# Kernel tuning notes

Measured on AMD Instinct MI355X. Metric: run time of the kernel, lower is better.

Reference implementation:

```python
import jax, jax.numpy as jnp
import numpy as np

B, S, HID = 2, 2048, 2048
N_HEADS, N_KV, HEAD_DIM = 8, 1, 256
ROPE_THETA = 10000.0
NEG = -1e9


def setup_inputs() -> dict:
    key = jax.random.key(0)
    ks = jax.random.split(key, 6)
    hidden_states = jax.random.normal(ks[0], (B, S, HID), dtype=jnp.float32)
    position_ids = jnp.broadcast_to(jnp.arange(S, dtype=jnp.int32)[None, :], (B, S))
    causal = jnp.tril(jnp.ones((S, S), dtype=bool))
    attention_mask = jnp.where(causal, 0.0, NEG).astype(jnp.float32)[None, None]
    attention_mask = jnp.broadcast_to(attention_mask, (B, 1, S, S))
    sc = 0.02
    Wq = jax.random.normal(ks[1], (N_HEADS * HEAD_DIM, HID), dtype=jnp.float32) * sc
    Wk = jax.random.normal(ks[2], (N_KV * HEAD_DIM, HID), dtype=jnp.float32) * sc
    Wv = jax.random.normal(ks[3], (N_KV * HEAD_DIM, HID), dtype=jnp.float32) * sc
    Wo = jax.random.normal(ks[4], (HID, N_HEADS * HEAD_DIM), dtype=jnp.float32) * sc
    return {"hidden_states": hidden_states, "position_ids": position_ids,
            "attention_mask": attention_mask, "Wq": Wq, "Wk": Wk, "Wv": Wv, "Wo": Wo}


def _rotate_half(x):
    x1, x2 = jnp.split(x, 2, axis=-1)
    return jnp.concatenate((-x2, x1), axis=-1)


def _rope_cos_sin(position_ids, head_dim, dtype):
    inv_freq = 1.0 / (ROPE_THETA ** (jnp.arange(0, head_dim, 2, dtype=jnp.float32) / head_dim))
    freqs = position_ids.astype(jnp.float32)[:, :, None] * inv_freq[None, None, :]  # [B,S,D/2]
    emb = jnp.concatenate((freqs, freqs), axis=-1)  # [B,S,D]
    return jnp.cos(emb).astype(dtype), jnp.sin(emb).astype(dtype)


def reference(hidden_states, position_ids, attention_mask, Wq, Wk, Wv, Wo):
    b, s, _ = hidden_states.shape
    d = HEAD_DIM
    rep = N_HEADS // N_KV
    q = (hidden_states @ Wq.T).reshape(b, s, N_HEADS, d).transpose(0, 2, 1, 3)  # [B,H,S,D]
    k = (hidden_states @ Wk.T).reshape(b, s, N_KV, d).transpose(0, 2, 1, 3)    # [B,KV,S,D]
    v = (hidden_states @ Wv.T).reshape(b, s, N_KV, d).transpose(0, 2, 1, 3)
    cos, sin = _rope_cos_sin(position_ids, d, hidden_states.dtype)
    cos, sin = cos[:, None], sin[:, None]  # broadcast over heads
    q = q * cos + _rotate_half(q) * sin
    k = k * cos + _rotate_half(k) * sin
    # GQA: group queries per kv head, no materialized repeat
    qg = q.reshape(b, N_KV, rep, s, d)
    scores = jnp.einsum('bgrqd,bgkd->bgrqk', qg, k) / jnp.sqrt(jnp.float32(d)).astype(q.dtype)
    scores = scores.reshape(b, N_HEADS, s, s) + attention_mask
    probs = jax.nn.softmax(scores.astype(jnp.float32), axis=-1).astype(q.dtype)
    out = jnp.einsum('bgrqk,bgkd->bgrqd', probs.reshape(b, N_KV, rep, s, s), v)
    out = out.reshape(b, N_HEADS, s, d).transpose(0, 2, 1, 3).reshape(b, s, N_HEADS * d)
    return out @ Wo.T
```

## Files before the change

### kernel.cpp

```cpp
#include <hip/hip_runtime.h>
#include <hip/hip_bf16.h>

typedef __bf16 bf16x8 __attribute__((ext_vector_type(8)));
typedef float  f32x4  __attribute__((ext_vector_type(4)));

#define BATCH 2
#define SEQ   2048
#define HID   2048
#define NH    8
#define DH    256
#define LQ    2560
#define ROWS  (BATCH*SEQ)
#define KVB   32
#define NQC   128

__device__ __forceinline__ void gld16(const void* g, void* l) {
    __builtin_amdgcn_global_load_lds(
        (__attribute__((address_space(1))) void*)(g),
        (__attribute__((address_space(3))) void*)(l), 16, 0, 0);
}

__device__ __forceinline__ unsigned pack2bf(float a, float b) {
    union { __bf16 h[2]; unsigned u; } x;
    x.h[0] = (__bf16)a; x.h[1] = (__bf16)b;
    return x.u;
}

__global__ void cvt_f32_bf16(const float* __restrict__ src, __bf16* __restrict__ dst, int n4) {
    int i = blockIdx.x * blockDim.x + threadIdx.x;
    if (i < n4) {
        float4 v = ((const float4*)src)[i];
        __bf16 o[4];
        o[0] = (__bf16)v.x; o[1] = (__bf16)v.y; o[2] = (__bf16)v.z; o[3] = (__bf16)v.w;
        ((uint2*)dst)[i] = *(uint2*)o;
    }
}

template<typename CT>
__global__ __launch_bounds__(256)
void gemm_bt(const __bf16* __restrict__ A, const __bf16* __restrict__ B,
             CT* __restrict__ C, int M, int N, int K) {
    __shared__ __bf16 sA[128 * 32];
    __shared__ __bf16 sB[128 * 32];
    const int tid  = threadIdx.x;
    const int lane = tid & 63;
    const int wid  = tid >> 6;
    const int row0 = blockIdx.y * 128;
    const int col0 = blockIdx.x * 128;
    const int wr = (wid >> 1) * 64;
    const int wc = (wid & 1) * 64;

    const int sr0 = tid >> 2, sc0 = (tid & 3) * 8;
    const __bf16* Ag0 = A + (size_t)(row0 + sr0) * K + sc0;
    const __bf16* Ag1 = Ag0 + (size_t)64 * K;
    const __bf16* Bg0 = B + (size_t)(col0 + sr0) * K + sc0;
    const __bf16* Bg1 = Bg0 + (size_t)64 * K;
    __bf16* lA0 = &sA[wid * 512];
    __bf16* lA1 = &sA[2048 + wid * 512];
    __bf16* lB0 = &sB[wid * 512];
    __bf16* lB1 = &sB[2048 + wid * 512];

    f32x4 acc[4][4];
#pragma unroll
    for (int m = 0; m < 4; ++m)
#pragma unroll
        for (int n = 0; n < 4; ++n) acc[m][n] = (f32x4)0.f;

    for (int k0 = 0; k0 < K; k0 += 32) {
        gld16(Ag0 + k0, lA0);
        gld16(Ag1 + k0, lA1);
        gld16(Bg0 + k0, lB0);
        gld16(Bg1 + k0, lB1);
        __syncthreads();
        bf16x8 af[4], bfr[4];
#pragma unroll
        for (int m = 0; m < 4; ++m)
            af[m] = *(const bf16x8*)&sA[(wr + m * 16 + (lane & 15)) * 32 + (lane >> 4) * 8];
#pragma unroll
        for (int n = 0; n < 4; ++n)
            bfr[n] = *(const bf16x8*)&sB[(wc + n * 16 + (lane & 15)) * 32 + (lane >> 4) * 8];
#pragma unroll
        for (int m = 0; m < 4; ++m)
#pragma unroll
            for (int n = 0; n < 4; ++n)
                acc[m][n] = __builtin_amdgcn_mfma_f32_16x16x32_bf16(af[m], bfr[n], acc[m][n], 0, 0, 0);
        __syncthreads();
    }
#pragma unroll
    for (int m = 0; m < 4; ++m)
#pragma unroll
        for (int n = 0; n < 4; ++n)
#pragma unroll
            for (int r = 0; r < 4; ++r) {
                int row = row0 + wr + m * 16 + (lane >> 4) * 4 + r;
                int col = col0 + wc + n * 16 + (lane & 15);
                C[(size_t)row * N + col] = (CT)acc[m][n][r];
            }
}

__global__ void rope_kernel(__bf16* __restrict__ QKV, const int* __restrict__ pid) {
    const int row = blockIdx.x;
    const int h   = blockIdx.y;
    const int j   = threadIdx.x;
    const float pos = (float)pid[row];
    const float freq = exp2f((float)j * (-13.287712379549449f / 128.0f));
    const float ang = pos * freq;
    float sn, cs;
    sincosf(ang, &sn, &cs);
    __bf16* p = QKV + (size_t)row * LQ + h * 256 + j;
    float x1 = (float)p[0], x2 = (float)p[128];
    p[0]   = (__bf16)(x1 * cs - x2 * sn);
    p[128] = (__bf16)(x2 * cs + x1 * sn);
}

__global__ __launch_bounds__(256)
void transpose_v(const __bf16* __restrict__ QKV, __bf16* __restrict__ Vt) {
    __shared__ __bf16 t[32][33];
    const int b  = blockIdx.z;
    const int s0 = blockIdx.x * 32;
    const int d0 = blockIdx.y * 32;
    const int c  = threadIdx.x & 31;
    const int r8 = threadIdx.x >> 5;
#pragma unroll
    for (int i = 0; i < 4; ++i) {
        int row = r8 + i * 8;
        t[row][c] = QKV[(size_t)(b * SEQ + s0 + row) * LQ + 2304 + d0 + c];
    }
    __syncthreads();
#pragma unroll
    for (int i = 0; i < 4; ++i) {
        int row = r8 + i * 8;
        Vt[((size_t)b * 256 + d0 + row) * SEQ + s0 + c] = t[c][row];
    }
}

__global__ __launch_bounds__(128, 2)
void attn_fwd2(const __bf16* __restrict__ QKV, const __bf16* __restrict__ Vt,
               __bf16* __restrict__ O) {
    __shared__ __bf16 Kt[2][KVB * 256];
    __shared__ __bf16 Vs[2][256 * KVB];

    const int tid  = threadIdx.x;
    const int lane = tid & 63;
    const int wid  = tid >> 6;
    const int lc   = lane & 15;
    const int l4   = lane >> 4;

    const int bid = blockIdx.x;
    const int hg  = bid & 3;
    const int p   = bid >> 2;
    const int b   = p >> 6;
    const int pr  = p & 63;
    const int h   = hg * 2 + wid;

    const char* QKVb = (const char*)(QKV + (size_t)(b * SEQ) * LQ);
    const char* Kg   = QKVb + 2048 * 2;
    const char* Vg   = (const char*)(Vt + (size_t)b * DH * SEQ);

    const int krow = wid * 16 + (lane >> 5);
    const int kcol = (lane & 31) * 16;
    const int vrow = wid * 128 + (lane >> 2);
    const int vcol = (lane & 3) * 16;

    for (int half = 0; half < 2; ++half) {
        const int qt = half ? (NQC - 1 - pr) : pr;
        const int q0 = qt * 16;
        const int nt = (qt >> 1) + 1;
        const int qrow = q0 + lc;

        const char* Qp = QKVb + (size_t)(q0 + lc) * (LQ * 2) + h * 512 + l4 * 16;
        bf16x8 qf[8];
#pragma unroll
        for (int kc = 0; kc < 8; ++kc) qf[kc] = *(const bf16x8*)(Qp + kc * 64);

        f32x4 oacc[16];
#pragma unroll
        for (int i = 0; i < 16; ++i) oacc[i] = (f32x4)0.f;
        float mrow = -1e30f, lrow = 0.f;

#pragma unroll
        for (int i = 0; i < 8; ++i) {
            int r = krow + i * 2;
            gld16(Kg + (size_t)r * (LQ * 2) + (kcol ^ ((r & 7) << 4)),
                  (char*)&Kt[0][0] + wid * 8192 + i * 1024);
        }
#pragma unroll
        for (int i = 0; i < 8; ++i) {
            int r = vrow + i * 16;
            gld16(Vg + (size_t)r * (SEQ * 2) + vcol,
                  (char*)&Vs[0][0] + wid * 8192 + i * 1024);
        }

        int buf = 0;
        for (int t = 0; t < nt; ++t) {
            __syncthreads();
            const int kv0 = t * KVB;
            if (t + 1 < nt) {
                const int kvn = kv0 + KVB;
#pragma unroll
                for (int i = 0; i < 8; ++i) {
                    int r = krow + i * 2;
                    gld16(Kg + (size_t)(kvn + r) * (LQ * 2) + (kcol ^ ((r & 7) << 4)),
                          (char*)&Kt[buf ^ 1][0] + wid * 8192 + i * 1024);
                }
#pragma unroll
                for (int i = 0; i < 8; ++i) {
                    int r = vrow + i * 16;
                    gld16(Vg + (size_t)r * (SEQ * 2) + kvn * 2 + vcol,
                          (char*)&Vs[buf ^ 1][0] + wid * 8192 + i * 1024);
                }
            }

            f32x4 sacc[2];
            sacc[0] = (f32x4)0.f; sacc[1] = (f32x4)0.f;
            const char* Kl = (const char*)&Kt[buf][0];
#pragma unroll
            for (int ct = 0; ct < 2; ++ct) {
                const int rr = ct * 16 + lc;
                const int rbase = rr * 512;
                const int sw = (rr & 7) << 4;
#pragma unroll
                for (int kc = 0; kc < 8; ++kc) {
                    bf16x8 kf = *(const bf16x8*)(Kl + rbase + (((kc << 6) | (l4 << 4)) ^ sw));
                    sacc[ct] = __builtin_amdgcn_mfma_f32_16x16x32_bf16(kf, qf[kc], sacc[ct], 0, 0, 0);
                }
            }

            const bool lastt = (t == nt - 1);
            float sv[2][4];
            float rm = -1e30f;
#pragma unroll
            for (int ct = 0; ct < 2; ++ct)
#pragma unroll
                for (int r = 0; r < 4; ++r) {
                    float s = sacc[ct][r] * 0.0625f;
                    if (lastt) {
                        int kv = kv0 + ct * 16 + l4 * 4 + r;
                        if (kv > qrow) s = -1e30f;
                    }
                    sv[ct][r] = s;
                    rm = fmaxf(rm, s);
                }
            rm = fmaxf(rm, __shfl_xor(rm, 16, 64));
            rm = fmaxf(rm, __shfl_xor(rm, 32, 64));
            const float mnew  = fmaxf(mrow, rm);
            const float alpha = __expf(mrow - mnew);
            mrow = mnew;
            float p0[4], p1[4], ps = 0.f;
#pragma unroll
            for (int r = 0; r < 4; ++r) { p0[r] = __expf(sv[0][r] - mnew); ps += p0[r]; }
#pragma unroll
            for (int r = 0; r < 4; ++r) { p1[r] = __expf(sv[1][r] - mnew); ps += p1[r]; }
            ps += __shfl_xor(ps, 16, 64);
            ps += __shfl_xor(ps, 32, 64);
            lrow = lrow * alpha + ps;
#pragma unroll
            for (int dt = 0; dt < 16; ++dt) {
                oacc[dt][0] *= alpha; oacc[dt][1] *= alpha;
                oacc[dt][2] *= alpha; oacc[dt][3] *= alpha;
            }

            unsigned pkA0 = pack2bf(p0[0], p0[1]), pkA1 = pack2bf(p0[2], p0[3]);
            unsigned pkB0 = pack2bf(p1[0], p1[1]), pkB1 = pack2bf(p1[2], p1[3]);
            const int sl0 = lc + 16 * ((2 * l4) & 3);
            const int sl1 = lc + 16 * ((2 * l4 + 1) & 3);
            unsigned a0 = __shfl(pkA0, sl0, 64), a1 = __shfl(pkA1, sl0, 64);
            unsigned b0 = __shfl(pkB0, sl0, 64), b1 = __shfl(pkB1, sl0, 64);
            unsigned c0 = __shfl(pkA0, sl1, 64), c1 = __shfl(pkA1, sl1, 64);
            unsigned d0 = __shfl(pkB0, sl1, 64), d1 = __shfl(pkB1, sl1, 64);
            const bool hi = (l4 >= 2);
            union { unsigned u[4]; bf16x8 v; } pb;
            pb.u[0] = hi ? b0 : a0;
            pb.u[1] = hi ? b1 : a1;
            pb.u[2] = hi ? d0 : c0;
            pb.u[3] = hi ? d1 : c1;

            const char* Vl = (const char*)&Vs[buf][0];
#pragma unroll
            for (int dt = 0; dt < 16; ++dt) {
                bf16x8 vf = *(const bf16x8*)(Vl + (dt * 16 + lc) * 64 + l4 * 16);
                oacc[dt] = __builtin_amdgcn_mfma_f32_16x16x32_bf16(vf, pb.v, oacc[dt], 0, 0, 0);
            }
            buf ^= 1;
        }

        const float inv = 1.f / lrow;
        char* Op = (char*)O + ((size_t)(b * SEQ + q0 + lc) * HID + h * 256 + l4 * 4) * 2;
#pragma unroll
        for (int dt = 0; dt < 16; ++dt) {
            __bf16 o4[4];
            o4[0] = (__bf16)(oacc[dt][0] * inv);
            o4[1] = (__bf16)(oacc[dt][1] * inv);
            o4[2] = (__bf16)(oacc[dt][2] * inv);
            o4[3] = (__bf16)(oacc[dt][3] * inv);
            *(uint2*)(Op + dt * 32) = *(uint2*)o4;
        }
        __syncthreads();
    }
}

extern "C" void kernel_launch(void* const* d_in, const int* in_sizes, int n_in,
                              void* d_out, int out_size, void* d_ws, size_t ws_size,
                              hipStream_t stream) {
    const float* hs  = (const float*)d_in[0];
    const int*   pid = (const int*)d_in[1];
    const float* Wq  = (const float*)d_in[3];
    const float* Wk  = (const float*)d_in[4];
    const float* Wv  = (const float*)d_in[5];
    const float* Wo  = (const float*)d_in[6];
    float* out = (float*)d_out;

    char* ws = (char*)d_ws;
    __bf16* Xb   = (__bf16*)ws;                       ws += (size_t)ROWS * HID * 2;
    __bf16* Wqkv = (__bf16*)ws;                       ws += (size_t)LQ * HID * 2;
    __bf16* Wob  = (__bf16*)ws;                       ws += (size_t)HID * HID * 2;
    __bf16* QKV  = (__bf16*)ws;                       ws += (size_t)ROWS * LQ * 2;
    __bf16* Vt   = (__bf16*)ws;                       ws += (size_t)BATCH * DH * SEQ * 2;
    __bf16* Oat  = Xb;

    cvt_f32_bf16<<<(ROWS * HID / 4 + 255) / 256, 256, 0, stream>>>(hs, Xb, ROWS * HID / 4);
    cvt_f32_bf16<<<(HID * HID / 4 + 255) / 256, 256, 0, stream>>>(Wq, Wqkv, HID * HID / 4);
    cvt_f32_bf16<<<(DH * HID / 4 + 255) / 256, 256, 0, stream>>>(Wk, Wqkv + (size_t)2048 * HID, DH * HID / 4);
    cvt_f32_bf16<<<(DH * HID / 4 + 255) / 256, 256, 0, stream>>>(Wv, Wqkv + (size_t)2304 * HID, DH * HID / 4);
    cvt_f32_bf16<<<(HID * HID / 4 + 255) / 256, 256, 0, stream>>>(Wo, Wob, HID * HID / 4);

    gemm_bt<__bf16><<<dim3(LQ / 128, ROWS / 128), 256, 0, stream>>>(Xb, Wqkv, QKV, ROWS, LQ, HID);

    rope_kernel<<<dim3(ROWS, 9), 128, 0, stream>>>(QKV, pid);

    transpose_v<<<dim3(SEQ / 32, DH / 32, BATCH), 256, 0, stream>>>(QKV, Vt);

    attn_fwd2<<<dim3(512), 128, 0, stream>>>(QKV, Vt, Oat);

    gemm_bt<float><<<dim3(HID / 128, ROWS / 128), 256, 0, stream>>>(Oat, Wob, out, ROWS, HID, HID);
}
```

Baseline: 412.8 us.

## Process two query sub-tiles per wave in attention, reusing K/V fragments

The attention kernel now gives each wave 32 query rows as two 16-row sub-tiles, so every K and V fragment read from LDS feeds two MFMAs. The old two-pass causal pairing is replaced by a block mapping that splits heads across two grid halves and reverses tile order in the second half. The softmax scale is folded into the RoPE kernel for Q, and the online-softmax rescale is skipped when the running max grows by at most 8. It also adds V-tile LDS swizzling and s_setprio around the MFMA blocks. The cost is higher register pressure (launch bounds drop to one block per CU) and bf16 rounding of the pre-scaled Q.

```diff
diff --git a/kernel.cpp b/kernel.cpp
--- a/kernel.cpp
+++ b/kernel.cpp
@@ -12,7 +12,6 @@
 #define LQ    2560
 #define ROWS  (BATCH*SEQ)
 #define KVB   32
-#define NQC   128
 
 __device__ __forceinline__ void gld16(const void* g, void* l) {
     __builtin_amdgcn_global_load_lds(
@@ -107,10 +106,11 @@
     const float ang = pos * freq;
     float sn, cs;
     sincosf(ang, &sn, &cs);
+    const float sc = (h < 8) ? 0.0625f : 1.0f;
     __bf16* p = QKV + (size_t)row * LQ + h * 256 + j;
     float x1 = (float)p[0], x2 = (float)p[128];
-    p[0]   = (__bf16)(x1 * cs - x2 * sn);
-    p[128] = (__bf16)(x2 * cs + x1 * sn);
+    p[0]   = (__bf16)((x1 * cs - x2 * sn) * sc);
+    p[128] = (__bf16)((x2 * cs + x1 * sn) * sc);
 }
 
 __global__ __launch_bounds__(256)
@@ -134,8 +134,8 @@
     }
 }
 
-__global__ __launch_bounds__(128, 2)
-void attn_fwd2(const __bf16* __restrict__ QKV, const __bf16* __restrict__ Vt,
+__global__ __launch_bounds__(128, 1)
+void attn_fwd3(const __bf16* __restrict__ QKV, const __bf16* __restrict__ Vt,
                __bf16* __restrict__ O) {
     __shared__ __bf16 Kt[2][KVB * 256];
     __shared__ __bf16 Vs[2][256 * KVB];
@@ -147,11 +147,12 @@
     const int l4   = lane >> 4;
 
     const int bid = blockIdx.x;
-    const int hg  = bid & 3;
-    const int p   = bid >> 2;
-    const int b   = p >> 6;
-    const int pr  = p & 63;
-    const int h   = hg * 2 + wid;
+    int qt, b, hg;
+    if (bid < 256) { qt = bid & 63;        b = (bid >> 6) & 1; hg = (bid >> 7) & 1; }
+    else { int r = bid - 256; qt = 63 - (r & 63); b = (r >> 6) & 1; hg = 2 + ((r >> 7) & 1); }
+    const int h  = hg * 2 + wid;
+    const int q0 = qt * 32;
+    const int nt = qt + 1;
 
     const char* QKVb = (const char*)(QKV + (size_t)(b * SEQ) * LQ);
     const char* Kg   = QKVb + 2048 * 2;
@@ -160,105 +161,115 @@
     const int krow = wid * 16 + (lane >> 5);
     const int kcol = (lane & 31) * 16;
     const int vrow = wid * 128 + (lane >> 2);
-    const int vcol = (lane & 3) * 16;
-
-    for (int half = 0; half < 2; ++half) {
-        const int qt = half ? (NQC - 1 - pr) : pr;
-        const int q0 = qt * 16;
-        const int nt = (qt >> 1) + 1;
-        const int qrow = q0 + lc;
-
-        const char* Qp = QKVb + (size_t)(q0 + lc) * (LQ * 2) + h * 512 + l4 * 16;
-        bf16x8 qf[8];
-#pragma unroll
-        for (int kc = 0; kc < 8; ++kc) qf[kc] = *(const bf16x8*)(Qp + kc * 64);
-
-        f32x4 oacc[16];
-#pragma unroll
-        for (int i = 0; i < 16; ++i) oacc[i] = (f32x4)0.f;
-        float mrow = -1e30f, lrow = 0.f;
-
-#pragma unroll
-        for (int i = 0; i < 8; ++i) {
-            int r = krow + i * 2;
-            gld16(Kg + (size_t)r * (LQ * 2) + (kcol ^ ((r & 7) << 4)),
-                  (char*)&Kt[0][0] + wid * 8192 + i * 1024);
-        }
-#pragma unroll
-        for (int i = 0; i < 8; ++i) {
-            int r = vrow + i * 16;
-            gld16(Vg + (size_t)r * (SEQ * 2) + vcol,
-                  (char*)&Vs[0][0] + wid * 8192 + i * 1024);
-        }
-
-        int buf = 0;
-        for (int t = 0; t < nt; ++t) {
-            __syncthreads();
-            const int kv0 = t * KVB;
-            if (t + 1 < nt) {
-                const int kvn = kv0 + KVB;
-#pragma unroll
-                for (int i = 0; i < 8; ++i) {
-                    int r = krow + i * 2;
-                    gld16(Kg + (size_t)(kvn + r) * (LQ * 2) + (kcol ^ ((r & 7) << 4)),
-                          (char*)&Kt[buf ^ 1][0] + wid * 8192 + i * 1024);
-                }
-#pragma unroll
-                for (int i = 0; i < 8; ++i) {
-                    int r = vrow + i * 16;
-                    gld16(Vg + (size_t)r * (SEQ * 2) + kvn * 2 + vcol,
-                          (char*)&Vs[buf ^ 1][0] + wid * 8192 + i * 1024);
-                }
-            }
-
-            f32x4 sacc[2];
-            sacc[0] = (f32x4)0.f; sacc[1] = (f32x4)0.f;
-            const char* Kl = (const char*)&Kt[buf][0];
-#pragma unroll
-            for (int ct = 0; ct < 2; ++ct) {
-                const int rr = ct * 16 + lc;
-                const int rbase = rr * 512;
-                const int sw = (rr & 7) << 4;
-#pragma unroll
-                for (int kc = 0; kc < 8; ++kc) {
-                    bf16x8 kf = *(const bf16x8*)(Kl + rbase + (((kc << 6) | (l4 << 4)) ^ sw));
-                    sacc[ct] = __builtin_amdgcn_mfma_f32_16x16x32_bf16(kf, qf[kc], sacc[ct], 0, 0, 0);
-                }
-            }
-
-            const bool lastt = (t == nt - 1);
-            float sv[2][4];
-            float rm = -1e30f;
+    const int vcol = ((lane & 3) * 16) ^ (((vrow >> 1) & 3) << 4);
+    const int vrsw = ((lc >> 1) & 3) << 4;
+
+    bf16x8 qf[2][8];
+#pragma unroll
+    for (int qs = 0; qs < 2; ++qs) {
+        const char* Qp = QKVb + (size_t)(q0 + qs * 16 + lc) * (LQ * 2) + h * 512 + l4 * 16;
+#pragma unroll
+        for (int kc = 0; kc < 8; ++kc) qf[qs][kc] = *(const bf16x8*)(Qp + kc * 64);
+    }
+
+    f32x4 oacc[2][16];
+#pragma unroll
+    for (int qs = 0; qs < 2; ++qs)
+#pragma unroll
+        for (int i = 0; i < 16; ++i) oacc[qs][i] = (f32x4)0.f;
+    float mrow[2] = {-1e30f, -1e30f}, lrow[2] = {0.f, 0.f};
+
+#pragma unroll
+    for (int i = 0; i < 8; ++i) {
+        int r = krow + i * 2;
+        gld16(Kg + (size_t)r * (LQ * 2) + (kcol ^ ((r & 7) << 4)),
+              (char*)&Kt[0][0] + wid * 8192 + i * 1024);
+    }
+#pragma unroll
+    for (int i = 0; i < 8; ++i) {
+        int r = vrow + i * 16;
+        gld16(Vg + (size_t)r * (SEQ * 2) + vcol,
+              (char*)&Vs[0][0] + wid * 8192 + i * 1024);
+    }
+
+    int buf = 0;
+    for (int t = 0; t < nt; ++t) {
+        __syncthreads();
+        const int kv0 = t * KVB;
+        if (t + 1 < nt) {
+            const int kvn = kv0 + KVB;
+#pragma unroll
+            for (int i = 0; i < 8; ++i) {
+                int r = krow + i * 2;
+                gld16(Kg + (size_t)(kvn + r) * (LQ * 2) + (kcol ^ ((r & 7) << 4)),
+                      (char*)&Kt[buf ^ 1][0] + wid * 8192 + i * 1024);
+            }
+#pragma unroll
+            for (int i = 0; i < 8; ++i) {
+                int r = vrow + i * 16;
+                gld16(Vg + (size_t)r * (SEQ * 2) + kvn * 2 + vcol,
+                      (char*)&Vs[buf ^ 1][0] + wid * 8192 + i * 1024);
+            }
+        }
+
+        f32x4 sacc[2][2];
+        sacc[0][0] = (f32x4)0.f; sacc[0][1] = (f32x4)0.f;
+        sacc[1][0] = (f32x4)0.f; sacc[1][1] = (f32x4)0.f;
+        const char* Kl = (const char*)&Kt[buf][0];
+        __builtin_amdgcn_s_setprio(1);
+#pragma unroll
+        for (int ct = 0; ct < 2; ++ct) {
+            const int rr = ct * 16 + lc;
+            const int rbase = rr * 512;
+            const int sw = (rr & 7) << 4;
+#pragma unroll
+            for (int kc = 0; kc < 8; ++kc) {
+                bf16x8 kf = *(const bf16x8*)(Kl + rbase + (((kc << 6) | (l4 << 4)) ^ sw));
+                sacc[0][ct] = __builtin_amdgcn_mfma_f32_16x16x32_bf16(kf, qf[0][kc], sacc[0][ct], 0, 0, 0);
+                sacc[1][ct] = __builtin_amdgcn_mfma_f32_16x16x32_bf16(kf, qf[1][kc], sacc[1][ct], 0, 0, 0);
+            }
+        }
+        __builtin_amdgcn_s_setprio(0);
+
+        const bool lastt = (t == nt - 1);
+        bf16x8 pbv[2];
+#pragma unroll
+        for (int qs = 0; qs < 2; ++qs) {
+            const int qrow = q0 + qs * 16 + lc;
+            float tm = -1e30f;
 #pragma unroll
             for (int ct = 0; ct < 2; ++ct)
 #pragma unroll
                 for (int r = 0; r < 4; ++r) {
-                    float s = sacc[ct][r] * 0.0625f;
+                    float s = sacc[qs][ct][r];
                     if (lastt) {
                         int kv = kv0 + ct * 16 + l4 * 4 + r;
                         if (kv > qrow) s = -1e30f;
                     }
-                    sv[ct][r] = s;
-                    rm = fmaxf(rm, s);
+                    sacc[qs][ct][r] = s;
+                    tm = fmaxf(tm, s);
                 }
-            rm = fmaxf(rm, __shfl_xor(rm, 16, 64));
-            rm = fmaxf(rm, __shfl_xor(rm, 32, 64));
-            const float mnew  = fmaxf(mrow, rm);
-            const float alpha = __expf(mrow - mnew);
-            mrow = mnew;
+            tm = fmaxf(tm, __shfl_xor(tm, 16, 64));
+            tm = fmaxf(tm, __shfl_xor(tm, 32, 64));
+            if (!__all(tm <= mrow[qs] + 8.f)) {
+                const float mnew  = fmaxf(mrow[qs], tm);
+                const float alpha = __expf(mrow[qs] - mnew);
+                mrow[qs] = mnew;
+                lrow[qs] *= alpha;
+#pragma unroll
+                for (int dt = 0; dt < 16; ++dt) {
+                    oacc[qs][dt][0] *= alpha; oacc[qs][dt][1] *= alpha;
+                    oacc[qs][dt][2] *= alpha; oacc[qs][dt][3] *= alpha;
+                }
+            }
             float p0[4], p1[4], ps = 0.f;
 #pragma unroll
-            for (int r = 0; r < 4; ++r) { p0[r] = __expf(sv[0][r] - mnew); ps += p0[r]; }
-#pragma unroll
-            for (int r = 0; r < 4; ++r) { p1[r] = __expf(sv[1][r] - mnew); ps += p1[r]; }
+            for (int r = 0; r < 4; ++r) { p0[r] = __expf(sacc[qs][0][r] - mrow[qs]); ps += p0[r]; }
+#pragma unroll
+            for (int r = 0; r < 4; ++r) { p1[r] = __expf(sacc[qs][1][r] - mrow[qs]); ps += p1[r]; }
             ps += __shfl_xor(ps, 16, 64);
             ps += __shfl_xor(ps, 32, 64);
-            lrow = lrow * alpha + ps;
-#pragma unroll
-            for (int dt = 0; dt < 16; ++dt) {
-                oacc[dt][0] *= alpha; oacc[dt][1] *= alpha;
-                oacc[dt][2] *= alpha; oacc[dt][3] *= alpha;
-            }
+            lrow[qs] += ps;
 
             unsigned pkA0 = pack2bf(p0[0], p0[1]), pkA1 = pack2bf(p0[2], p0[3]);
             unsigned pkB0 = pack2bf(p1[0], p1[1]), pkB1 = pack2bf(p1[2], p1[3]);
@@ -274,28 +285,34 @@
             pb.u[1] = hi ? b1 : a1;
             pb.u[2] = hi ? d0 : c0;
             pb.u[3] = hi ? d1 : c1;
-
-            const char* Vl = (const char*)&Vs[buf][0];
-#pragma unroll
-            for (int dt = 0; dt < 16; ++dt) {
-                bf16x8 vf = *(const bf16x8*)(Vl + (dt * 16 + lc) * 64 + l4 * 16);
-                oacc[dt] = __builtin_amdgcn_mfma_f32_16x16x32_bf16(vf, pb.v, oacc[dt], 0, 0, 0);
-            }
-            buf ^= 1;
-        }
-
-        const float inv = 1.f / lrow;
-        char* Op = (char*)O + ((size_t)(b * SEQ + q0 + lc) * HID + h * 256 + l4 * 4) * 2;
+            pbv[qs] = pb.v;
+        }
+
+        const char* Vl = (const char*)&Vs[buf][0];
+        __builtin_amdgcn_s_setprio(1);
+#pragma unroll
+        for (int dt = 0; dt < 16; ++dt) {
+            bf16x8 vf = *(const bf16x8*)(Vl + (dt * 16 + lc) * 64 + ((l4 << 4) ^ vrsw));
+            oacc[0][dt] = __builtin_amdgcn_mfma_f32_16x16x32_bf16(vf, pbv[0], oacc[0][dt], 0, 0, 0);
+            oacc[1][dt] = __builtin_amdgcn_mfma_f32_16x16x32_bf16(vf, pbv[1], oacc[1][dt], 0, 0, 0);
+        }
+        __builtin_amdgcn_s_setprio(0);
+        buf ^= 1;
+    }
+
+#pragma unroll
+    for (int qs = 0; qs < 2; ++qs) {
+        const float inv = 1.f / lrow[qs];
+        char* Op = (char*)O + ((size_t)(b * SEQ + q0 + qs * 16 + lc) * HID + h * 256 + l4 * 4) * 2;
 #pragma unroll
         for (int dt = 0; dt < 16; ++dt) {
             __bf16 o4[4];
-            o4[0] = (__bf16)(oacc[dt][0] * inv);
-            o4[1] = (__bf16)(oacc[dt][1] * inv);
-            o4[2] = (__bf16)(oacc[dt][2] * inv);
-            o4[3] = (__bf16)(oacc[dt][3] * inv);
+            o4[0] = (__bf16)(oacc[qs][dt][0] * inv);
+            o4[1] = (__bf16)(oacc[qs][dt][1] * inv);
+            o4[2] = (__bf16)(oacc[qs][dt][2] * inv);
+            o4[3] = (__bf16)(oacc[qs][dt][3] * inv);
             *(uint2*)(Op + dt * 32) = *(uint2*)o4;
         }
-        __syncthreads();
     }
 }
 
@@ -330,7 +347,7 @@
 
     transpose_v<<<dim3(SEQ / 32, DH / 32, BATCH), 256, 0, stream>>>(QKV, Vt);
 
-    attn_fwd2<<<dim3(512), 128, 0, stream>>>(QKV, Vt, Oat);
+    attn_fwd3<<<dim3(512), 128, 0, stream>>>(QKV, Vt, Oat);
 
     gemm_bt<float><<<dim3(HID / 128, ROWS / 128), 256, 0, stream>>>(Oat, Wob, out, ROWS, HID, HID);
 }
```

New measurement: 428.6 us. 3.8% more time.

## Share K/V tiles across all 8 heads per block in attention

Applied to the files above, without the earlier changes.

The attention kernel now uses 512-thread blocks with one wave per head, so all 8 query heads of a 16-row query tile share each staged K/V tile. The old scheme split heads across 4 blocks and paired causal tiles for load balance. The change also folds the 1/16 softmax scale into RoPE for Q heads, swizzles the V shared-memory layout to avoid bank conflicts, and raises wave priority around the MFMA loops. It adds a lazy rescale that skips the running-max update unless the max grows by more than 8. Giving up the causal half-pairing leaves 256 blocks of uneven length, which may cost load balance.

```diff
diff --git a/kernel.cpp b/kernel.cpp
--- a/kernel.cpp
+++ b/kernel.cpp
@@ -12,7 +12,6 @@
 #define LQ    2560
 #define ROWS  (BATCH*SEQ)
 #define KVB   32
-#define NQC   128
 
 __device__ __forceinline__ void gld16(const void* g, void* l) {
     __builtin_amdgcn_global_load_lds(
@@ -107,10 +106,11 @@
     const float ang = pos * freq;
     float sn, cs;
     sincosf(ang, &sn, &cs);
+    const float sc = (h < 8) ? 0.0625f : 1.0f;
     __bf16* p = QKV + (size_t)row * LQ + h * 256 + j;
     float x1 = (float)p[0], x2 = (float)p[128];
-    p[0]   = (__bf16)(x1 * cs - x2 * sn);
-    p[128] = (__bf16)(x2 * cs + x1 * sn);
+    p[0]   = (__bf16)((x1 * cs - x2 * sn) * sc);
+    p[128] = (__bf16)((x2 * cs + x1 * sn) * sc);
 }
 
 __global__ __launch_bounds__(256)
@@ -134,8 +134,8 @@
     }
 }
 
-__global__ __launch_bounds__(128, 2)
-void attn_fwd2(const __bf16* __restrict__ QKV, const __bf16* __restrict__ Vt,
+__global__ __launch_bounds__(512, 2)
+void attn_fwd4(const __bf16* __restrict__ QKV, const __bf16* __restrict__ Vt,
                __bf16* __restrict__ O) {
     __shared__ __bf16 Kt[2][KVB * 256];
     __shared__ __bf16 Vs[2][256 * KVB];
@@ -147,156 +147,146 @@
     const int l4   = lane >> 4;
 
     const int bid = blockIdx.x;
-    const int hg  = bid & 3;
-    const int p   = bid >> 2;
-    const int b   = p >> 6;
-    const int pr  = p & 63;
-    const int h   = hg * 2 + wid;
+    const int b   = bid >> 7;
+    const int qt  = bid & 127;
+    const int q0  = qt * 16;
+    const int nt  = (qt >> 1) + 1;
+    const int h   = wid;
 
     const char* QKVb = (const char*)(QKV + (size_t)(b * SEQ) * LQ);
     const char* Kg   = QKVb + 2048 * 2;
     const char* Vg   = (const char*)(Vt + (size_t)b * DH * SEQ);
 
-    const int krow = wid * 16 + (lane >> 5);
-    const int kcol = (lane & 31) * 16;
-    const int vrow = wid * 128 + (lane >> 2);
-    const int vcol = (lane & 3) * 16;
-
-    for (int half = 0; half < 2; ++half) {
-        const int qt = half ? (NQC - 1 - pr) : pr;
-        const int q0 = qt * 16;
-        const int nt = (qt >> 1) + 1;
-        const int qrow = q0 + lc;
-
-        const char* Qp = QKVb + (size_t)(q0 + lc) * (LQ * 2) + h * 512 + l4 * 16;
-        bf16x8 qf[8];
-#pragma unroll
-        for (int kc = 0; kc < 8; ++kc) qf[kc] = *(const bf16x8*)(Qp + kc * 64);
-
-        f32x4 oacc[16];
-#pragma unroll
-        for (int i = 0; i < 16; ++i) oacc[i] = (f32x4)0.f;
-        float mrow = -1e30f, lrow = 0.f;
-
-#pragma unroll
-        for (int i = 0; i < 8; ++i) {
-            int r = krow + i * 2;
-            gld16(Kg + (size_t)r * (LQ * 2) + (kcol ^ ((r & 7) << 4)),
-                  (char*)&Kt[0][0] + wid * 8192 + i * 1024);
-        }
-#pragma unroll
-        for (int i = 0; i < 8; ++i) {
-            int r = vrow + i * 16;
-            gld16(Vg + (size_t)r * (SEQ * 2) + vcol,
-                  (char*)&Vs[0][0] + wid * 8192 + i * 1024);
-        }
-
-        int buf = 0;
-        for (int t = 0; t < nt; ++t) {
-            __syncthreads();
-            const int kv0 = t * KVB;
-            if (t + 1 < nt) {
-                const int kvn = kv0 + KVB;
-#pragma unroll
-                for (int i = 0; i < 8; ++i) {
-                    int r = krow + i * 2;
-                    gld16(Kg + (size_t)(kvn + r) * (LQ * 2) + (kcol ^ ((r & 7) << 4)),
-                          (char*)&Kt[buf ^ 1][0] + wid * 8192 + i * 1024);
-                }
-#pragma unroll
-                for (int i = 0; i < 8; ++i) {
-                    int r = vrow + i * 16;
-                    gld16(Vg + (size_t)r * (SEQ * 2) + kvn * 2 + vcol,
-                          (char*)&Vs[buf ^ 1][0] + wid * 8192 + i * 1024);
-                }
-            }
-
-            f32x4 sacc[2];
-            sacc[0] = (f32x4)0.f; sacc[1] = (f32x4)0.f;
-            const char* Kl = (const char*)&Kt[buf][0];
+    const int kr0   = wid * 4 + (lane >> 5);
+    const int kcolb = (lane & 31) * 16;
+    const int vd0   = wid * 32 + (lane >> 2);
+    const int vcol0 = (lane & 3) * 16;
+    const int vrsw  = ((lc >> 1) & 3) << 4;
+
+#define STAGE(B_, KV0) do {                                                         \
+    _Pragma("unroll")                                                               \
+    for (int i_ = 0; i_ < 2; ++i_) {                                                \
+        int r_ = kr0 + i_ * 2;                                                      \
+        gld16(Kg + (size_t)((KV0) + r_) * (LQ * 2) + (kcolb ^ ((r_ & 7) << 4)),     \
+              (char*)&Kt[B_][0] + (wid * 2 + i_) * 1024);                           \
+    }                                                                               \
+    _Pragma("unroll")                                                               \
+    for (int i_ = 0; i_ < 2; ++i_) {                                                \
+        int d_ = vd0 + i_ * 16;                                                     \
+        gld16(Vg + (size_t)d_ * (SEQ * 2) + (KV0) * 2 + (vcol0 ^ (((d_ >> 1) & 3) << 4)), \
+              (char*)&Vs[B_][0] + (wid * 2 + i_) * 1024);                           \
+    }                                                                               \
+} while (0)
+
+    const char* Qp = QKVb + (size_t)(q0 + lc) * (LQ * 2) + h * 512 + l4 * 16;
+    bf16x8 qf[8];
+#pragma unroll
+    for (int kc = 0; kc < 8; ++kc) qf[kc] = *(const bf16x8*)(Qp + kc * 64);
+
+    f32x4 oacc[16];
+#pragma unroll
+    for (int i = 0; i < 16; ++i) oacc[i] = (f32x4)0.f;
+    float mrow = -1e30f, lrow = 0.f;
+    const int qrow = q0 + lc;
+
+    STAGE(0, 0);
+
+    int buf = 0;
+    for (int t = 0; t < nt; ++t) {
+        __syncthreads();
+        const int kv0 = t * KVB;
+        if (t + 1 < nt) STAGE(buf ^ 1, kv0 + KVB);
+
+        f32x4 sacc[2];
+        sacc[0] = (f32x4)0.f; sacc[1] = (f32x4)0.f;
+        const char* Kl = (const char*)&Kt[buf][0];
+        __builtin_amdgcn_s_setprio(1);
+#pragma unroll
+        for (int kc = 0; kc < 8; ++kc) {
 #pragma unroll
             for (int ct = 0; ct < 2; ++ct) {
                 const int rr = ct * 16 + lc;
-                const int rbase = rr * 512;
-                const int sw = (rr & 7) << 4;
-#pragma unroll
-                for (int kc = 0; kc < 8; ++kc) {
-                    bf16x8 kf = *(const bf16x8*)(Kl + rbase + (((kc << 6) | (l4 << 4)) ^ sw));
-                    sacc[ct] = __builtin_amdgcn_mfma_f32_16x16x32_bf16(kf, qf[kc], sacc[ct], 0, 0, 0);
+                bf16x8 kf = *(const bf16x8*)(Kl + rr * 512 +
+                                             (((kc << 6) | (l4 << 4)) ^ ((rr & 7) << 4)));
+                sacc[ct] = __builtin_amdgcn_mfma_f32_16x16x32_bf16(kf, qf[kc], sacc[ct], 0, 0, 0);
+            }
+        }
+        __builtin_amdgcn_s_setprio(0);
+
+        const bool lastt = (t == nt - 1);
+        float tm = -1e30f;
+#pragma unroll
+        for (int ct = 0; ct < 2; ++ct)
+#pragma unroll
+            for (int r = 0; r < 4; ++r) {
+                float s = sacc[ct][r];
+                if (lastt) {
+                    int kv = kv0 + ct * 16 + l4 * 4 + r;
+                    if (kv > qrow) s = -1e30f;
                 }
+                sacc[ct][r] = s;
+                tm = fmaxf(tm, s);
             }
-
-            const bool lastt = (t == nt - 1);
-            float sv[2][4];
-            float rm = -1e30f;
-#pragma unroll
-            for (int ct = 0; ct < 2; ++ct)
-#pragma unroll
-                for (int r = 0; r < 4; ++r) {
-                    float s = sacc[ct][r] * 0.0625f;
-                    if (lastt) {
-                        int kv = kv0 + ct * 16 + l4 * 4 + r;
-                        if (kv > qrow) s = -1e30f;
-                    }
-                    sv[ct][r] = s;
-                    rm = fmaxf(rm, s);
-                }
-            rm = fmaxf(rm, __shfl_xor(rm, 16, 64));
-            rm = fmaxf(rm, __shfl_xor(rm, 32, 64));
-            const float mnew  = fmaxf(mrow, rm);
+        tm = fmaxf(tm, __shfl_xor(tm, 16, 64));
+        tm = fmaxf(tm, __shfl_xor(tm, 32, 64));
+        if (!__all(tm <= mrow + 8.f)) {
+            const float mnew  = fmaxf(mrow, tm);
             const float alpha = __expf(mrow - mnew);
             mrow = mnew;
-            float p0[4], p1[4], ps = 0.f;
-#pragma unroll
-            for (int r = 0; r < 4; ++r) { p0[r] = __expf(sv[0][r] - mnew); ps += p0[r]; }
-#pragma unroll
-            for (int r = 0; r < 4; ++r) { p1[r] = __expf(sv[1][r] - mnew); ps += p1[r]; }
-            ps += __shfl_xor(ps, 16, 64);
-            ps += __shfl_xor(ps, 32, 64);
-            lrow = lrow * alpha + ps;
+            lrow *= alpha;
 #pragma unroll
             for (int dt = 0; dt < 16; ++dt) {
                 oacc[dt][0] *= alpha; oacc[dt][1] *= alpha;
                 oacc[dt][2] *= alpha; oacc[dt][3] *= alpha;
             }
-
-            unsigned pkA0 = pack2bf(p0[0], p0[1]), pkA1 = pack2bf(p0[2], p0[3]);
-            unsigned pkB0 = pack2bf(p1[0], p1[1]), pkB1 = pack2bf(p1[2], p1[3]);
-            const int sl0 = lc + 16 * ((2 * l4) & 3);
-            const int sl1 = lc + 16 * ((2 * l4 + 1) & 3);
-            unsigned a0 = __shfl(pkA0, sl0, 64), a1 = __shfl(pkA1, sl0, 64);
-            unsigned b0 = __shfl(pkB0, sl0, 64), b1 = __shfl(pkB1, sl0, 64);
-            unsigned c0 = __shfl(pkA0, sl1, 64), c1 = __shfl(pkA1, sl1, 64);
-            unsigned d0 = __shfl(pkB0, sl1, 64), d1 = __shfl(pkB1, sl1, 64);
-            const bool hi = (l4 >= 2);
-            union { unsigned u[4]; bf16x8 v; } pb;
-            pb.u[0] = hi ? b0 : a0;
-            pb.u[1] = hi ? b1 : a1;
-            pb.u[2] = hi ? d0 : c0;
-            pb.u[3] = hi ? d1 : c1;
-
-            const char* Vl = (const char*)&Vs[buf][0];
-#pragma unroll
-            for (int dt = 0; dt < 16; ++dt) {
-                bf16x8 vf = *(const bf16x8*)(Vl + (dt * 16 + lc) * 64 + l4 * 16);
-                oacc[dt] = __builtin_amdgcn_mfma_f32_16x16x32_bf16(vf, pb.v, oacc[dt], 0, 0, 0);
-            }
-            buf ^= 1;
         }
-
-        const float inv = 1.f / lrow;
-        char* Op = (char*)O + ((size_t)(b * SEQ + q0 + lc) * HID + h * 256 + l4 * 4) * 2;
+        float p0[4], p1[4], ps = 0.f;
+#pragma unroll
+        for (int r = 0; r < 4; ++r) { p0[r] = __expf(sacc[0][r] - mrow); ps += p0[r]; }
+#pragma unroll
+        for (int r = 0; r < 4; ++r) { p1[r] = __expf(sacc[1][r] - mrow); ps += p1[r]; }
+        ps += __shfl_xor(ps, 16, 64);
+        ps += __shfl_xor(ps, 32, 64);
+        lrow += ps;
+
+        unsigned pkA0 = pack2bf(p0[0], p0[1]), pkA1 = pack2bf(p0[2], p0[3]);
+        unsigned pkB0 = pack2bf(p1[0], p1[1]), pkB1 = pack2bf(p1[2], p1[3]);
+        const int sl0 = lc + 16 * ((2 * l4) & 3);
+        const int sl1 = lc + 16 * ((2 * l4 + 1) & 3);
+        unsigned a0 = __shfl(pkA0, sl0, 64), a1 = __shfl(pkA1, sl0, 64);
+        unsigned b0 = __shfl(pkB0, sl0, 64), b1 = __shfl(pkB1, sl0, 64);
+        unsigned c0 = __shfl(pkA0, sl1, 64), c1 = __shfl(pkA1, sl1, 64);
+        unsigned d0 = __shfl(pkB0, sl1, 64), d1 = __shfl(pkB1, sl1, 64);
+        const bool hi = (l4 >= 2);
+        union { unsigned u[4]; bf16x8 v; } pb;
+        pb.u[0] = hi ? b0 : a0;
+        pb.u[1] = hi ? b1 : a1;
+        pb.u[2] = hi ? d0 : c0;
+        pb.u[3] = hi ? d1 : c1;
+
+        const char* Vl = (const char*)&Vs[buf][0];
+        __builtin_amdgcn_s_setprio(1);
 #pragma unroll
         for (int dt = 0; dt < 16; ++dt) {
-            __bf16 o4[4];
-            o4[0] = (__bf16)(oacc[dt][0] * inv);
-            o4[1] = (__bf16)(oacc[dt][1] * inv);
-            o4[2] = (__bf16)(oacc[dt][2] * inv);
-            o4[3] = (__bf16)(oacc[dt][3] * inv);
-            *(uint2*)(Op + dt * 32) = *(uint2*)o4;
+            bf16x8 vf = *(const bf16x8*)(Vl + (dt * 16 + lc) * 64 + ((l4 << 4) ^ vrsw));
+            oacc[dt] = __builtin_amdgcn_mfma_f32_16x16x32_bf16(vf, pb.v, oacc[dt], 0, 0, 0);
         }
-        __syncthreads();
-    }
+        __builtin_amdgcn_s_setprio(0);
+        buf ^= 1;
+    }
+
+    const float inv = 1.f / lrow;
+    char* Op = (char*)O + ((size_t)(b * SEQ + q0 + lc) * HID + h * 256 + l4 * 4) * 2;
+#pragma unroll
+    for (int dt = 0; dt < 16; ++dt) {
+        __bf16 o4[4];
+        o4[0] = (__bf16)(oacc[dt][0] * inv);
+        o4[1] = (__bf16)(oacc[dt][1] * inv);
+        o4[2] = (__bf16)(oacc[dt][2] * inv);
+        o4[3] = (__bf16)(oacc[dt][3] * inv);
+        *(uint2*)(Op + dt * 32) = *(uint2*)o4;
+    }
+#undef STAGE
 }
 
 extern "C" void kernel_launch(void* const* d_in, const int* in_sizes, int n_in,
@@ -330,7 +320,7 @@
 
     transpose_v<<<dim3(SEQ / 32, DH / 32, BATCH), 256, 0, stream>>>(QKV, Vt);
 
-    attn_fwd2<<<dim3(512), 128, 0, stream>>>(QKV, Vt, Oat);
+    attn_fwd4<<<dim3(256), 512, 0, stream>>>(QKV, Vt, Oat);
 
     gemm_bt<float><<<dim3(HID / 128, ROWS / 128), 256, 0, stream>>>(Oat, Wob, out, ROWS, HID, HID);
 }
```

After: 393.5 us. 1.05x faster.
